# Kernel optimization log

Measured on AMD Instinct MI355X. Metric: run time of the kernel, lower is better.

The kernel has to match this reference:

```python
import jax, jax.numpy as jnp
import numpy as np

NEG_SLOPE = 0.01  # nn.LeakyReLU() default; module's alpha=-0.2 is unused
MASK_VAL = -1e12

N, IN_DIM, OUT_DIM = 4096, 512, 64


def setup_inputs() -> dict:
    key = jax.random.key(0)
    k1, k2, k3, k4 = jax.random.split(key, 4)
    input_h = jax.random.normal(k1, (N, IN_DIM), dtype=jnp.float32)
    adj = jax.random.randint(k2, (N, N), 0, 2, dtype=jnp.int32)
    W = jax.random.normal(k3, (IN_DIM, OUT_DIM), dtype=jnp.float32) * 0.05
    a = jax.random.normal(k4, (2 * OUT_DIM, 1), dtype=jnp.float32) * 0.05
    return {"input_h": input_h, "adj": adj, "W": W, "a": a}


def reference(input_h, adj, W, a):
    h = input_h @ W  # [N, D]
    D = h.shape[1]
    # e_ij = leakyrelu(a^T [h_i || h_j]) = leakyrelu(a1.h_i + a2.h_j)
    a1, a2 = a[:D, 0], a[D:, 0]
    s1 = h @ a1  # [N]
    s2 = h @ a2  # [N]
    e = s1[:, None] + s2[None, :]  # [N, N]
    e = jnp.where(e >= 0, e, NEG_SLOPE * e)  # LeakyReLU(0.01)
    scores = jnp.where(adj > 0, e, MASK_VAL)
    attention = jax.nn.softmax(scores, axis=1)
    # dropout omitted (eval mode / deterministic reference)
    return attention @ h  # [N, D]
```

## Files before the change

kernel.cpp:

```cpp
#include <hip/hip_runtime.h>
#include <hip/hip_bf16.h>

#define NN 4096
#define IN_DIM 512
#define OUT_D 64
#define LOG2E 1.44269504088896340736f

typedef __attribute__((ext_vector_type(8))) short short8v;
typedef __attribute__((ext_vector_type(4))) float f32x4;

__device__ __forceinline__ short to_bf16_rne(float x) {
  unsigned u = __builtin_bit_cast(unsigned, x);
  u = (u + 0x7FFFu + ((u >> 16) & 1u)) >> 16;
  return (short)u;
}
__device__ __forceinline__ float bf16_to_f(short h) {
  unsigned u = ((unsigned)(unsigned short)h) << 16;
  return __builtin_bit_cast(float, u);
}

__global__ __launch_bounds__(256) void k_cvt(
    const float* __restrict__ X, short* __restrict__ Xhi, short* __restrict__ Xlo)
{
  int idx = blockIdx.x * 256 + threadIdx.x;
  const float* p = X + (size_t)idx * 8;
  float4 v0 = *(const float4*)(p);
  float4 v1 = *(const float4*)(p + 4);
  float f[8]; *(float4*)f = v0; *(float4*)(f + 4) = v1;
  short8v hi, lo;
  #pragma unroll
  for (int r = 0; r < 8; ++r) {
    short h = to_bf16_rne(f[r]);
    hi[r] = h;
    lo[r] = to_bf16_rne(f[r] - bf16_to_f(h));
  }
  *(short8v*)(Xhi + (size_t)idx * 8) = hi;
  *(short8v*)(Xlo + (size_t)idx * 8) = lo;
}

__global__ __launch_bounds__(256) void k_wpack(
    const float* __restrict__ W, short* __restrict__ Ahi, short* __restrict__ Alo)
{
  int tid = blockIdx.x * 256 + threadIdx.x;
  int l = tid & 63, t = (tid >> 6) & 15, m = tid >> 10;
  int dd = m * 16 + (l & 15);
  int kbase = t * 32 + 8 * (l >> 4);
  short8v hi, lo;
  #pragma unroll
  for (int r = 0; r < 8; ++r) {
    float w = W[(size_t)(kbase + r) * OUT_D + dd];
    short h = to_bf16_rne(w);
    hi[r] = h;
    lo[r] = to_bf16_rne(w - bf16_to_f(h));
  }
  *(short8v*)(Ahi + (size_t)tid * 8) = hi;
  *(short8v*)(Alo + (size_t)tid * 8) = lo;
}

__global__ __launch_bounds__(256) void k_h_mfma(
    const short* __restrict__ Xhi, const short* __restrict__ Xlo,
    const short* __restrict__ Ahi, const short* __restrict__ Alo,
    const float* __restrict__ a,
    short* __restrict__ hbT, float* __restrict__ s1, float* __restrict__ s2)
{
  __shared__ float sm1[4][16], sm2[4][16];
  int m = threadIdx.x >> 6;
  int l = threadIdx.x & 63;
  int lo = l & 15, g = l >> 4;
  int row0 = blockIdx.x * 16;

  f32x4 acc = {0.f, 0.f, 0.f, 0.f};
  const short* xh = Xhi + (size_t)(row0 + lo) * IN_DIM + g * 8;
  const short* xl = Xlo + (size_t)(row0 + lo) * IN_DIM + g * 8;
  const short* ah = Ahi + ((size_t)(m * 16) * 64 + l) * 8;
  const short* al = Alo + ((size_t)(m * 16) * 64 + l) * 8;

  #pragma unroll
  for (int t = 0; t < 16; ++t) {
    short8v bhi = *(const short8v*)(xh + t * 32);
    short8v blo = *(const short8v*)(xl + t * 32);
    short8v fhi = *(const short8v*)(ah + (size_t)t * 64 * 8);
    short8v flo = *(const short8v*)(al + (size_t)t * 64 * 8);
    acc = __builtin_amdgcn_mfma_f32_16x16x32_bf16(fhi, bhi, acc, 0, 0, 0);
    acc = __builtin_amdgcn_mfma_f32_16x16x32_bf16(fhi, blo, acc, 0, 0, 0);
    acc = __builtin_amdgcn_mfma_f32_16x16x32_bf16(flo, bhi, acc, 0, 0, 0);
  }

  float p1 = 0.f, p2 = 0.f;
  #pragma unroll
  for (int q = 0; q < 4; ++q) {
    int d = m * 16 + 4 * g + q;
    hbT[(size_t)d * NN + row0 + lo] = to_bf16_rne(acc[q]);
    p1 = fmaf(acc[q], a[d], p1);
    p2 = fmaf(acc[q], a[OUT_D + d], p2);
  }
  p1 += __shfl_xor(p1, 16); p1 += __shfl_xor(p1, 32);
  p2 += __shfl_xor(p2, 16); p2 += __shfl_xor(p2, 32);
  if (l < 16) { sm1[m][l] = p1; sm2[m][l] = p2; }
  __syncthreads();
  if (threadIdx.x < 16) {
    int r = threadIdx.x;
    s1[row0 + r] = (sm1[0][r] + sm1[1][r] + sm1[2][r] + sm1[3][r]) * LOG2E;
    s2[row0 + r] = (sm2[0][r] + sm2[1][r] + sm2[2][r] + sm2[3][r]) * LOG2E;
  }
}

__global__ __launch_bounds__(256) void k_h(
    const float* __restrict__ X, const float* __restrict__ W,
    const float* __restrict__ a,
    short* __restrict__ hbT, float* __restrict__ s1, float* __restrict__ s2)
{
  int tid = threadIdx.x;
  int dp = tid & 31;
  int rw = tid >> 5;
  int row = blockIdx.x * 8 + rw;
  const float* xrow = X + (size_t)row * IN_DIM;
  int d = dp * 2;
  float acc0 = 0.f, acc1 = 0.f;
  #pragma unroll 4
  for (int k4 = 0; k4 < IN_DIM / 4; ++k4) {
    float4 xv = *(const float4*)(xrow + k4 * 4);
    float2 w0 = *(const float2*)(W + (k4 * 4 + 0) * OUT_D + d);
    float2 w1 = *(const float2*)(W + (k4 * 4 + 1) * OUT_D + d);
    float2 w2 = *(const float2*)(W + (k4 * 4 + 2) * OUT_D + d);
    float2 w3 = *(const float2*)(W + (k4 * 4 + 3) * OUT_D + d);
    acc0 = fmaf(xv.x, w0.x, acc0); acc1 = fmaf(xv.x, w0.y, acc1);
    acc0 = fmaf(xv.y, w1.x, acc0); acc1 = fmaf(xv.y, w1.y, acc1);
    acc0 = fmaf(xv.z, w2.x, acc0); acc1 = fmaf(xv.z, w2.y, acc1);
    acc0 = fmaf(xv.w, w3.x, acc0); acc1 = fmaf(xv.w, w3.y, acc1);
  }
  hbT[(size_t)d * NN + row]       = to_bf16_rne(acc0);
  hbT[(size_t)(d + 1) * NN + row] = to_bf16_rne(acc1);
  float p1 = a[d] * acc0 + a[d + 1] * acc1;
  float p2 = a[OUT_D + d] * acc0 + a[OUT_D + d + 1] * acc1;
  #pragma unroll
  for (int off = 16; off >= 1; off >>= 1) {
    p1 += __shfl_xor(p1, off);
    p2 += __shfl_xor(p2, off);
  }
  if (dp == 0) { s1[row] = p1 * LOG2E; s2[row] = p2 * LOG2E; }
}

__global__ __launch_bounds__(256) void k_s2max(const float* __restrict__ s2,
                                               float* __restrict__ s2max)
{
  __shared__ float red[256];
  float m = -3.0e38f;
  for (int i = threadIdx.x; i < NN; i += 256) m = fmaxf(m, s2[i]);
  red[threadIdx.x] = m;
  __syncthreads();
  for (int s = 128; s > 0; s >>= 1) {
    if ((int)threadIdx.x < s) red[threadIdx.x] = fmaxf(red[threadIdx.x], red[threadIdx.x + s]);
    __syncthreads();
  }
  if (threadIdx.x == 0) *s2max = red[0];
}

__global__ __launch_bounds__(256) void k_attn(
    const int* __restrict__ adj, const short* __restrict__ hbT,
    const float* __restrict__ s1, const float* __restrict__ s2,
    const float* __restrict__ s2maxp,
    float* __restrict__ accp, float* __restrict__ lpart, int jchunk)
{
  int w  = threadIdx.x >> 6;
  int l  = threadIdx.x & 63;
  int lo = l & 15, g = l >> 4;
  int part  = blockIdx.y;
  int ibase = blockIdx.x * 64 + w * 16;
  int row   = ibase + lo;

  float s1v = s1[row];
  float x = s1v + *s2maxp;
  float M = fmaxf(x, 0.01f * x);

  f32x4 c0 = {0.f,0.f,0.f,0.f}, c1 = {0.f,0.f,0.f,0.f};
  f32x4 c2 = {0.f,0.f,0.f,0.f}, c3 = {0.f,0.f,0.f,0.f};
  float lsum = 0.f;

  const int* adjrow = adj + (size_t)row * NN;
  int j0 = part * jchunk;
  int jj = j0 + g * 8;

  int4  pa0 = *(const int4*)(adjrow + jj);
  int4  pa1 = *(const int4*)(adjrow + jj + 4);
  float4 ps0 = *(const float4*)(s2 + jj);
  float4 ps1 = *(const float4*)(s2 + jj + 4);

  for (int js = 0; js < jchunk; js += 32) {
    int4 a0 = pa0, a1 = pa1;
    float4 t0 = ps0, t1 = ps1;
    int jn = jj + 32;
    if (js + 32 < jchunk) {
      pa0 = *(const int4*)(adjrow + jn);
      pa1 = *(const int4*)(adjrow + jn + 4);
      ps0 = *(const float4*)(s2 + jn);
      ps1 = *(const float4*)(s2 + jn + 4);
    }

    short8v b0 = *(const short8v*)(hbT + ((size_t)(lo)      << 12) + jj);
    short8v b1 = *(const short8v*)(hbT + ((size_t)(16 + lo) << 12) + jj);
    short8v b2 = *(const short8v*)(hbT + ((size_t)(32 + lo) << 12) + jj);
    short8v b3 = *(const short8v*)(hbT + ((size_t)(48 + lo) << 12) + jj);

    int av[8]; float sv[8];
    *(int4*)(av) = a0;  *(int4*)(av + 4) = a1;
    *(float4*)(sv) = t0; *(float4*)(sv + 4) = t1;

    short8v af;
    #pragma unroll
    for (int r = 0; r < 8; ++r) {
      float y = s1v + sv[r];
      float e = fmaxf(y, 0.01f * y);
      float p = exp2f(e - M);
      p = (av[r] > 0) ? p : 0.f;
      lsum += p;
      af[r] = to_bf16_rne(p);
    }

    c0 = __builtin_amdgcn_mfma_f32_16x16x32_bf16(af, b0, c0, 0, 0, 0);
    c1 = __builtin_amdgcn_mfma_f32_16x16x32_bf16(af, b1, c1, 0, 0, 0);
    c2 = __builtin_amdgcn_mfma_f32_16x16x32_bf16(af, b2, c2, 0, 0, 0);
    c3 = __builtin_amdgcn_mfma_f32_16x16x32_bf16(af, b3, c3, 0, 0, 0);
    jj = jn;
  }

  lsum += __shfl_xor(lsum, 16);
  lsum += __shfl_xor(lsum, 32);
  if (l < 16) lpart[(size_t)part * NN + ibase + l] = lsum;

  float* ap = accp + ((size_t)part * NN + ibase) * OUT_D;
  #pragma unroll
  for (int q = 0; q < 4; ++q) {
    int ri = g * 4 + q;
    ap[ri * OUT_D +  0 + lo] = c0[q];
    ap[ri * OUT_D + 16 + lo] = c1[q];
    ap[ri * OUT_D + 32 + lo] = c2[q];
    ap[ri * OUT_D + 48 + lo] = c3[q];
  }
}

__global__ __launch_bounds__(256) void k_combine(
    const float* __restrict__ accp, const float* __restrict__ lpart,
    float* __restrict__ out, int npart)
{
  int idx = blockIdx.x * 256 + threadIdx.x;
  int i = idx >> 6;
  float s = 0.f, li = 0.f;
  for (int p = 0; p < npart; ++p) {
    s  += accp[(size_t)p * (NN * OUT_D) + idx];
    li += lpart[(size_t)p * NN + i];
  }
  out[idx] = s / li;
}

extern "C" void kernel_launch(void* const* d_in, const int* in_sizes, int n_in,
                              void* d_out, int out_size, void* d_ws, size_t ws_size,
                              hipStream_t stream)
{
  const float* X   = (const float*)d_in[0];
  const int*   adj = (const int*)d_in[1];
  const float* W   = (const float*)d_in[2];
  const float* a   = (const float*)d_in[3];
  float* out = (float*)d_out;

  char* ws = (char*)d_ws;
  size_t off = 0;
  float* s1  = (float*)(ws + off); off += NN * 4;
  float* s2  = (float*)(ws + off); off += NN * 4;
  float* s2m = (float*)(ws + off); off += 64;
  short* hbT = (short*)(ws + off); off += (size_t)OUT_D * NN * 2;
  size_t fixed_old = off;

  short* Xhi = (short*)(ws + off); off += (size_t)NN * IN_DIM * 2;
  short* Xlo = (short*)(ws + off); off += (size_t)NN * IN_DIM * 2;
  short* Ahi = (short*)(ws + off); off += 4096 * 8 * 2;
  short* Alo = (short*)(ws + off); off += 4096 * 8 * 2;
  size_t fixed_new = off;

  size_t per_part = (size_t)(NN * OUT_D + NN) * 4;
  int npart = 0; bool use_mfma = true;
  for (int p = 8; p >= 1; p >>= 1)
    if (fixed_new + (size_t)p * per_part <= ws_size) { npart = p; break; }
  if (npart == 0) {
    use_mfma = false;
    for (int p = 8; p >= 1; p >>= 1)
      if (fixed_old + (size_t)p * per_part <= ws_size) { npart = p; break; }
    if (npart == 0) npart = 1;
  }
  char* base2 = ws + (use_mfma ? fixed_new : fixed_old);
  float* accp  = (float*)base2;
  float* lpart = (float*)(base2 + (size_t)npart * NN * OUT_D * 4);
  int jchunk = NN / npart;

  if (use_mfma) {
    k_cvt<<<(NN * IN_DIM) / (8 * 256), 256, 0, stream>>>(X, Xhi, Xlo);
    k_wpack<<<16, 256, 0, stream>>>(W, Ahi, Alo);
    k_h_mfma<<<NN / 16, 256, 0, stream>>>(Xhi, Xlo, Ahi, Alo, a, hbT, s1, s2);
  } else {
    k_h<<<NN / 8, 256, 0, stream>>>(X, W, a, hbT, s1, s2);
  }
  k_s2max<<<1, 256, 0, stream>>>(s2, s2m);
  dim3 grid_attn(NN / 64, npart);
  k_attn<<<grid_attn, 256, 0, stream>>>(adj, hbT, s1, s2, s2m, accp, lpart, jchunk);
  k_combine<<<(NN * OUT_D) / 256, 256, 0, stream>>>(accp, lpart, out, npart);
}
```

Before: 54.06 us.

## Fuse X conversion into projection, atomic s2 max, templated deeper-prefetch attention

Removes the separate fp32-to-bf16 hi/lo conversion kernel: the projection kernel now loads X directly, splits it into swizzled shared memory, and also reduces s2's max through an order-preserving atomicMax key. This drops the k_cvt and single-block k_s2max launches along with the Xhi/Xlo workspace traffic. The attention kernel is templated on chunk size with a two-deep register prefetch, and npart can rise to 16 for more parallelism. The trade-off is a larger combine pass and more partial-sum memory.

```diff
diff --git a/kernel.cpp b/kernel.cpp
--- a/kernel.cpp
+++ b/kernel.cpp
@@ -18,30 +18,21 @@
   unsigned u = ((unsigned)(unsigned short)h) << 16;
   return __builtin_bit_cast(float, u);
 }
-
-__global__ __launch_bounds__(256) void k_cvt(
-    const float* __restrict__ X, short* __restrict__ Xhi, short* __restrict__ Xlo)
-{
-  int idx = blockIdx.x * 256 + threadIdx.x;
-  const float* p = X + (size_t)idx * 8;
-  float4 v0 = *(const float4*)(p);
-  float4 v1 = *(const float4*)(p + 4);
-  float f[8]; *(float4*)f = v0; *(float4*)(f + 4) = v1;
-  short8v hi, lo;
-  #pragma unroll
-  for (int r = 0; r < 8; ++r) {
-    short h = to_bf16_rne(f[r]);
-    hi[r] = h;
-    lo[r] = to_bf16_rne(f[r] - bf16_to_f(h));
-  }
-  *(short8v*)(Xhi + (size_t)idx * 8) = hi;
-  *(short8v*)(Xlo + (size_t)idx * 8) = lo;
+__device__ __forceinline__ unsigned fkey(float f) {
+  unsigned u = __builtin_bit_cast(unsigned, f);
+  return u ^ ((unsigned)((int)u >> 31) | 0x80000000u);
+}
+__device__ __forceinline__ float funkey(unsigned k) {
+  unsigned u = (k >> 31) ? (k ^ 0x80000000u) : ~k;
+  return __builtin_bit_cast(float, u);
 }
 
 __global__ __launch_bounds__(256) void k_wpack(
-    const float* __restrict__ W, short* __restrict__ Ahi, short* __restrict__ Alo)
+    const float* __restrict__ W, short* __restrict__ Ahi, short* __restrict__ Alo,
+    unsigned* __restrict__ s2key)
 {
   int tid = blockIdx.x * 256 + threadIdx.x;
+  if (tid == 0) *s2key = 0u;
   int l = tid & 63, t = (tid >> 6) & 15, m = tid >> 10;
   int dd = m * 16 + (l & 15);
   int kbase = t * 32 + 8 * (l >> 4);
@@ -58,27 +49,49 @@
 }
 
 __global__ __launch_bounds__(256) void k_h_mfma(
-    const short* __restrict__ Xhi, const short* __restrict__ Xlo,
+    const float* __restrict__ X,
     const short* __restrict__ Ahi, const short* __restrict__ Alo,
     const float* __restrict__ a,
-    short* __restrict__ hbT, float* __restrict__ s1, float* __restrict__ s2)
-{
+    short* __restrict__ hbT, float* __restrict__ s1, float* __restrict__ s2,
+    unsigned* __restrict__ s2key)
+{
+  __shared__ short xhi[16 * 512];
+  __shared__ short xlo[16 * 512];
   __shared__ float sm1[4][16], sm2[4][16];
-  int m = threadIdx.x >> 6;
-  int l = threadIdx.x & 63;
-  int lo = l & 15, g = l >> 4;
+  int tid = threadIdx.x;
+  int m = tid >> 6, l = tid & 63, lo = l & 15, g = l >> 4;
   int row0 = blockIdx.x * 16;
 
+  #pragma unroll
+  for (int i = 0; i < 4; ++i) {
+    int flat = i * 2048 + tid * 8;
+    int r = flat >> 9, k = flat & 511;
+    float f[8];
+    *(float4*)(f)     = *(const float4*)(X + (size_t)row0 * IN_DIM + flat);
+    *(float4*)(f + 4) = *(const float4*)(X + (size_t)row0 * IN_DIM + flat + 4);
+    short8v hi, lov;
+    #pragma unroll
+    for (int q = 0; q < 8; ++q) {
+      short h = to_bf16_rne(f[q]);
+      hi[q] = h;
+      lov[q] = to_bf16_rne(f[q] - bf16_to_f(h));
+    }
+    int chunk = k >> 3;
+    int dst = (r << 9) + ((chunk ^ (r & 7)) << 3);
+    *(short8v*)(xhi + dst) = hi;
+    *(short8v*)(xlo + dst) = lov;
+  }
+  __syncthreads();
+
   f32x4 acc = {0.f, 0.f, 0.f, 0.f};
-  const short* xh = Xhi + (size_t)(row0 + lo) * IN_DIM + g * 8;
-  const short* xl = Xlo + (size_t)(row0 + lo) * IN_DIM + g * 8;
   const short* ah = Ahi + ((size_t)(m * 16) * 64 + l) * 8;
   const short* al = Alo + ((size_t)(m * 16) * 64 + l) * 8;
-
   #pragma unroll
   for (int t = 0; t < 16; ++t) {
-    short8v bhi = *(const short8v*)(xh + t * 32);
-    short8v blo = *(const short8v*)(xl + t * 32);
+    int c = t * 4 + g;
+    int src = (lo << 9) + ((c ^ (lo & 7)) << 3);
+    short8v bhi = *(const short8v*)(xhi + src);
+    short8v blo = *(const short8v*)(xlo + src);
     short8v fhi = *(const short8v*)(ah + (size_t)t * 64 * 8);
     short8v flo = *(const short8v*)(al + (size_t)t * 64 * 8);
     acc = __builtin_amdgcn_mfma_f32_16x16x32_bf16(fhi, bhi, acc, 0, 0, 0);
@@ -98,70 +111,26 @@
   p2 += __shfl_xor(p2, 16); p2 += __shfl_xor(p2, 32);
   if (l < 16) { sm1[m][l] = p1; sm2[m][l] = p2; }
   __syncthreads();
-  if (threadIdx.x < 16) {
-    int r = threadIdx.x;
-    s1[row0 + r] = (sm1[0][r] + sm1[1][r] + sm1[2][r] + sm1[3][r]) * LOG2E;
-    s2[row0 + r] = (sm2[0][r] + sm2[1][r] + sm2[2][r] + sm2[3][r]) * LOG2E;
-  }
-}
-
-__global__ __launch_bounds__(256) void k_h(
-    const float* __restrict__ X, const float* __restrict__ W,
-    const float* __restrict__ a,
-    short* __restrict__ hbT, float* __restrict__ s1, float* __restrict__ s2)
-{
-  int tid = threadIdx.x;
-  int dp = tid & 31;
-  int rw = tid >> 5;
-  int row = blockIdx.x * 8 + rw;
-  const float* xrow = X + (size_t)row * IN_DIM;
-  int d = dp * 2;
-  float acc0 = 0.f, acc1 = 0.f;
-  #pragma unroll 4
-  for (int k4 = 0; k4 < IN_DIM / 4; ++k4) {
-    float4 xv = *(const float4*)(xrow + k4 * 4);
-    float2 w0 = *(const float2*)(W + (k4 * 4 + 0) * OUT_D + d);
-    float2 w1 = *(const float2*)(W + (k4 * 4 + 1) * OUT_D + d);
-    float2 w2 = *(const float2*)(W + (k4 * 4 + 2) * OUT_D + d);
-    float2 w3 = *(const float2*)(W + (k4 * 4 + 3) * OUT_D + d);
-    acc0 = fmaf(xv.x, w0.x, acc0); acc1 = fmaf(xv.x, w0.y, acc1);
-    acc0 = fmaf(xv.y, w1.x, acc0); acc1 = fmaf(xv.y, w1.y, acc1);
-    acc0 = fmaf(xv.z, w2.x, acc0); acc1 = fmaf(xv.z, w2.y, acc1);
-    acc0 = fmaf(xv.w, w3.x, acc0); acc1 = fmaf(xv.w, w3.y, acc1);
-  }
-  hbT[(size_t)d * NN + row]       = to_bf16_rne(acc0);
-  hbT[(size_t)(d + 1) * NN + row] = to_bf16_rne(acc1);
-  float p1 = a[d] * acc0 + a[d + 1] * acc1;
-  float p2 = a[OUT_D + d] * acc0 + a[OUT_D + d + 1] * acc1;
-  #pragma unroll
-  for (int off = 16; off >= 1; off >>= 1) {
-    p1 += __shfl_xor(p1, off);
-    p2 += __shfl_xor(p2, off);
-  }
-  if (dp == 0) { s1[row] = p1 * LOG2E; s2[row] = p2 * LOG2E; }
-}
-
-__global__ __launch_bounds__(256) void k_s2max(const float* __restrict__ s2,
-                                               float* __restrict__ s2max)
-{
-  __shared__ float red[256];
-  float m = -3.0e38f;
-  for (int i = threadIdx.x; i < NN; i += 256) m = fmaxf(m, s2[i]);
-  red[threadIdx.x] = m;
-  __syncthreads();
-  for (int s = 128; s > 0; s >>= 1) {
-    if ((int)threadIdx.x < s) red[threadIdx.x] = fmaxf(red[threadIdx.x], red[threadIdx.x + s]);
-    __syncthreads();
-  }
-  if (threadIdx.x == 0) *s2max = red[0];
-}
-
+  if (tid < 16) {
+    float v1 = (sm1[0][tid] + sm1[1][tid] + sm1[2][tid] + sm1[3][tid]) * LOG2E;
+    float v2 = (sm2[0][tid] + sm2[1][tid] + sm2[2][tid] + sm2[3][tid]) * LOG2E;
+    s1[row0 + tid] = v1;
+    s2[row0 + tid] = v2;
+    float v = v2;
+    #pragma unroll
+    for (int off = 8; off >= 1; off >>= 1) v = fmaxf(v, __shfl_xor(v, off));
+    if (tid == 0) atomicMax(s2key, fkey(v));
+  }
+}
+
+template<int JCHUNK>
 __global__ __launch_bounds__(256) void k_attn(
     const int* __restrict__ adj, const short* __restrict__ hbT,
     const float* __restrict__ s1, const float* __restrict__ s2,
-    const float* __restrict__ s2maxp,
-    float* __restrict__ accp, float* __restrict__ lpart, int jchunk)
-{
+    const unsigned* __restrict__ s2keyp,
+    float* __restrict__ accp, float* __restrict__ lpart)
+{
+  constexpr int NIT = JCHUNK / 32;
   int w  = threadIdx.x >> 6;
   int l  = threadIdx.x & 63;
   int lo = l & 15, g = l >> 4;
@@ -170,7 +139,7 @@
   int row   = ibase + lo;
 
   float s1v = s1[row];
-  float x = s1v + *s2maxp;
+  float x = s1v + funkey(*s2keyp);
   float M = fmaxf(x, 0.01f * x);
 
   f32x4 c0 = {0.f,0.f,0.f,0.f}, c1 = {0.f,0.f,0.f,0.f};
@@ -178,29 +147,36 @@
   float lsum = 0.f;
 
   const int* adjrow = adj + (size_t)row * NN;
-  int j0 = part * jchunk;
-  int jj = j0 + g * 8;
-
-  int4  pa0 = *(const int4*)(adjrow + jj);
-  int4  pa1 = *(const int4*)(adjrow + jj + 4);
-  float4 ps0 = *(const float4*)(s2 + jj);
-  float4 ps1 = *(const float4*)(s2 + jj + 4);
-
-  for (int js = 0; js < jchunk; js += 32) {
-    int4 a0 = pa0, a1 = pa1;
-    float4 t0 = ps0, t1 = ps1;
-    int jn = jj + 32;
-    if (js + 32 < jchunk) {
-      pa0 = *(const int4*)(adjrow + jn);
-      pa1 = *(const int4*)(adjrow + jn + 4);
-      ps0 = *(const float4*)(s2 + jn);
-      ps1 = *(const float4*)(s2 + jn + 4);
+  int jj = part * JCHUNK + g * 8;
+
+  int4 pa0[2], pa1[2]; float4 ps0[2], ps1[2];
+  #pragma unroll
+  for (int p = 0; p < 2; ++p) {
+    int j = jj + p * 32;
+    pa0[p] = *(const int4*)(adjrow + j);
+    pa1[p] = *(const int4*)(adjrow + j + 4);
+    ps0[p] = *(const float4*)(s2 + j);
+    ps1[p] = *(const float4*)(s2 + j + 4);
+  }
+
+  #pragma unroll
+  for (int it = 0; it < NIT; ++it) {
+    const int buf = it & 1;
+    int4 a0 = pa0[buf], a1 = pa1[buf];
+    float4 t0 = ps0[buf], t1 = ps1[buf];
+    if (it + 2 < NIT) {
+      int j = jj + (it + 2) * 32;
+      pa0[buf] = *(const int4*)(adjrow + j);
+      pa1[buf] = *(const int4*)(adjrow + j + 4);
+      ps0[buf] = *(const float4*)(s2 + j);
+      ps1[buf] = *(const float4*)(s2 + j + 4);
     }
-
-    short8v b0 = *(const short8v*)(hbT + ((size_t)(lo)      << 12) + jj);
-    short8v b1 = *(const short8v*)(hbT + ((size_t)(16 + lo) << 12) + jj);
-    short8v b2 = *(const short8v*)(hbT + ((size_t)(32 + lo) << 12) + jj);
-    short8v b3 = *(const short8v*)(hbT + ((size_t)(48 + lo) << 12) + jj);
+    int jc = jj + it * 32;
+
+    short8v b0 = *(const short8v*)(hbT + ((size_t)(lo)      << 12) + jc);
+    short8v b1 = *(const short8v*)(hbT + ((size_t)(16 + lo) << 12) + jc);
+    short8v b2 = *(const short8v*)(hbT + ((size_t)(32 + lo) << 12) + jc);
+    short8v b3 = *(const short8v*)(hbT + ((size_t)(48 + lo) << 12) + jc);
 
     int av[8]; float sv[8];
     *(int4*)(av) = a0;  *(int4*)(av + 4) = a1;
@@ -221,7 +197,6 @@
     c1 = __builtin_amdgcn_mfma_f32_16x16x32_bf16(af, b1, c1, 0, 0, 0);
     c2 = __builtin_amdgcn_mfma_f32_16x16x32_bf16(af, b2, c2, 0, 0, 0);
     c3 = __builtin_amdgcn_mfma_f32_16x16x32_bf16(af, b3, c3, 0, 0, 0);
-    jj = jn;
   }
 
   lsum += __shfl_xor(lsum, 16);
@@ -239,6 +214,67 @@
   }
 }
 
+__global__ __launch_bounds__(256) void k_attn_rt(
+    const int* __restrict__ adj, const short* __restrict__ hbT,
+    const float* __restrict__ s1, const float* __restrict__ s2,
+    const unsigned* __restrict__ s2keyp,
+    float* __restrict__ accp, float* __restrict__ lpart, int jchunk)
+{
+  int w  = threadIdx.x >> 6;
+  int l  = threadIdx.x & 63;
+  int lo = l & 15, g = l >> 4;
+  int part  = blockIdx.y;
+  int ibase = blockIdx.x * 64 + w * 16;
+  int row   = ibase + lo;
+  float s1v = s1[row];
+  float x = s1v + funkey(*s2keyp);
+  float M = fmaxf(x, 0.01f * x);
+  f32x4 c0 = {0.f,0.f,0.f,0.f}, c1 = {0.f,0.f,0.f,0.f};
+  f32x4 c2 = {0.f,0.f,0.f,0.f}, c3 = {0.f,0.f,0.f,0.f};
+  float lsum = 0.f;
+  const int* adjrow = adj + (size_t)row * NN;
+  int jj = part * jchunk + g * 8;
+  for (int js = 0; js < jchunk; js += 32, jj += 32) {
+    int4 a0 = *(const int4*)(adjrow + jj);
+    int4 a1 = *(const int4*)(adjrow + jj + 4);
+    float4 t0 = *(const float4*)(s2 + jj);
+    float4 t1 = *(const float4*)(s2 + jj + 4);
+    short8v b0 = *(const short8v*)(hbT + ((size_t)(lo)      << 12) + jj);
+    short8v b1 = *(const short8v*)(hbT + ((size_t)(16 + lo) << 12) + jj);
+    short8v b2 = *(const short8v*)(hbT + ((size_t)(32 + lo) << 12) + jj);
+    short8v b3 = *(const short8v*)(hbT + ((size_t)(48 + lo) << 12) + jj);
+    int av[8]; float sv[8];
+    *(int4*)(av) = a0;  *(int4*)(av + 4) = a1;
+    *(float4*)(sv) = t0; *(float4*)(sv + 4) = t1;
+    short8v af;
+    #pragma unroll
+    for (int r = 0; r < 8; ++r) {
+      float y = s1v + sv[r];
+      float e = fmaxf(y, 0.01f * y);
+      float p = exp2f(e - M);
+      p = (av[r] > 0) ? p : 0.f;
+      lsum += p;
+      af[r] = to_bf16_rne(p);
+    }
+    c0 = __builtin_amdgcn_mfma_f32_16x16x32_bf16(af, b0, c0, 0, 0, 0);
+    c1 = __builtin_amdgcn_mfma_f32_16x16x32_bf16(af, b1, c1, 0, 0, 0);
+    c2 = __builtin_amdgcn_mfma_f32_16x16x32_bf16(af, b2, c2, 0, 0, 0);
+    c3 = __builtin_amdgcn_mfma_f32_16x16x32_bf16(af, b3, c3, 0, 0, 0);
+  }
+  lsum += __shfl_xor(lsum, 16);
+  lsum += __shfl_xor(lsum, 32);
+  if (l < 16) lpart[(size_t)part * NN + ibase + l] = lsum;
+  float* ap = accp + ((size_t)part * NN + ibase) * OUT_D;
+  #pragma unroll
+  for (int q = 0; q < 4; ++q) {
+    int ri = g * 4 + q;
+    ap[ri * OUT_D +  0 + lo] = c0[q];
+    ap[ri * OUT_D + 16 + lo] = c1[q];
+    ap[ri * OUT_D + 32 + lo] = c2[q];
+    ap[ri * OUT_D + 48 + lo] = c3[q];
+  }
+}
+
 __global__ __launch_bounds__(256) void k_combine(
     const float* __restrict__ accp, const float* __restrict__ lpart,
     float* __restrict__ out, int npart)
@@ -267,40 +303,27 @@
   size_t off = 0;
   float* s1  = (float*)(ws + off); off += NN * 4;
   float* s2  = (float*)(ws + off); off += NN * 4;
-  float* s2m = (float*)(ws + off); off += 64;
+  unsigned* s2key = (unsigned*)(ws + off); off += 64;
   short* hbT = (short*)(ws + off); off += (size_t)OUT_D * NN * 2;
-  size_t fixed_old = off;
-
-  short* Xhi = (short*)(ws + off); off += (size_t)NN * IN_DIM * 2;
-  short* Xlo = (short*)(ws + off); off += (size_t)NN * IN_DIM * 2;
   short* Ahi = (short*)(ws + off); off += 4096 * 8 * 2;
   short* Alo = (short*)(ws + off); off += 4096 * 8 * 2;
-  size_t fixed_new = off;
+  size_t fixed = off;
 
   size_t per_part = (size_t)(NN * OUT_D + NN) * 4;
-  int npart = 0; bool use_mfma = true;
-  for (int p = 8; p >= 1; p >>= 1)
-    if (fixed_new + (size_t)p * per_part <= ws_size) { npart = p; break; }
-  if (npart == 0) {
-    use_mfma = false;
-    for (int p = 8; p >= 1; p >>= 1)
-      if (fixed_old + (size_t)p * per_part <= ws_size) { npart = p; break; }
-    if (npart == 0) npart = 1;
-  }
-  char* base2 = ws + (use_mfma ? fixed_new : fixed_old);
-  float* accp  = (float*)base2;
-  float* lpart = (float*)(base2 + (size_t)npart * NN * OUT_D * 4);
-  int jchunk = NN / npart;
-
-  if (use_mfma) {
-    k_cvt<<<(NN * IN_DIM) / (8 * 256), 256, 0, stream>>>(X, Xhi, Xlo);
-    k_wpack<<<16, 256, 0, stream>>>(W, Ahi, Alo);
-    k_h_mfma<<<NN / 16, 256, 0, stream>>>(Xhi, Xlo, Ahi, Alo, a, hbT, s1, s2);
-  } else {
-    k_h<<<NN / 8, 256, 0, stream>>>(X, W, a, hbT, s1, s2);
-  }
-  k_s2max<<<1, 256, 0, stream>>>(s2, s2m);
+  int npart = 1;
+  for (int p = 16; p >= 1; p >>= 1)
+    if (fixed + (size_t)p * per_part <= ws_size) { npart = p; break; }
+  float* accp  = (float*)(ws + fixed);
+  float* lpart = (float*)(ws + fixed + (size_t)npart * NN * OUT_D * 4);
+
+  k_wpack<<<16, 256, 0, stream>>>(W, Ahi, Alo, s2key);
+  k_h_mfma<<<NN / 16, 256, 0, stream>>>(X, Ahi, Alo, a, hbT, s1, s2, s2key);
   dim3 grid_attn(NN / 64, npart);
-  k_attn<<<grid_attn, 256, 0, stream>>>(adj, hbT, s1, s2, s2m, accp, lpart, jchunk);
+  if (npart == 16)
+    k_attn<256><<<grid_attn, 256, 0, stream>>>(adj, hbT, s1, s2, s2key, accp, lpart);
+  else if (npart == 8)
+    k_attn<512><<<grid_attn, 256, 0, stream>>>(adj, hbT, s1, s2, s2key, accp, lpart);
+  else
+    k_attn_rt<<<grid_attn, 256, 0, stream>>>(adj, hbT, s1, s2, s2key, accp, lpart, NN / npart);
   k_combine<<<(NN * OUT_D) / 256, 256, 0, stream>>>(accp, lpart, out, npart);
 }
```

After: 54.08 us. No clear change (+0.0%).
